# Kernel optimization log

Hardware: AMD Instinct MI355X
Metric: run time of the kernel (lower is better)

Reference implementation:

```python
import jax, jax.numpy as jnp
import numpy as np

D_MODEL = 1024
N_HEADS = 16
DK = D_MODEL // N_HEADS


def setup_inputs() -> dict:
    key = jax.random.key(0)
    k1, k2, k3, k4 = jax.random.split(key, 4)
    x = jax.random.normal(k1, (2, 2048, D_MODEL), dtype=jnp.float32)
    # torch nn.Linear stores weight as [out_features, in_features]
    W_qkv = jax.random.normal(k2, (3 * D_MODEL, D_MODEL), dtype=jnp.float32) * (1.0 / np.sqrt(D_MODEL))
    W_proj = jax.random.normal(k3, (D_MODEL, D_MODEL), dtype=jnp.float32) * (1.0 / np.sqrt(D_MODEL))
    b_proj = jax.random.normal(k4, (D_MODEL,), dtype=jnp.float32) * 0.01
    return {"x": x, "W_qkv": W_qkv, "W_proj": W_proj, "b_proj": b_proj}


def reference(x, W_qkv, W_proj, b_proj):
    B, L, D = x.shape
    qkv = x @ W_qkv.T                      # [B, L, 3D]
    q, k, v = jnp.split(qkv, 3, axis=-1)   # each [B, L, D]

    def split_heads(t):
        return t.reshape(B, L, N_HEADS, DK).transpose(0, 2, 1, 3)  # [B, H, L, dk]

    q, k, v = map(split_heads, (q, k, v))
    scale = jnp.float32(1.0 / np.sqrt(DK))
    scores = jnp.einsum('bhid,bhjd->bhij', q, k) * scale  # [B, H, L, L]
    attn = jax.nn.softmax(scores, axis=-1)
    out = jnp.einsum('bhij,bhjd->bhid', attn, v)           # [B, H, L, dk]
    out = out.transpose(0, 2, 1, 3).reshape(B, L, D)
    return out @ W_proj.T + b_proj
```

## Files before the change

### kernel.cpp

```cpp
#include <hip/hip_runtime.h>
#include <stdint.h>

typedef unsigned short ushort_t;
typedef __bf16 bf16x4 __attribute__((ext_vector_type(4)));
typedef __bf16 bf16x8 __attribute__((ext_vector_type(8)));
typedef float f32x4 __attribute__((ext_vector_type(4)));
typedef float f32x16 __attribute__((ext_vector_type(16)));
typedef unsigned short us8 __attribute__((ext_vector_type(8)));
typedef unsigned short us4v __attribute__((ext_vector_type(4)));

__device__ __forceinline__ float bf2f(ushort_t u) {
  union { uint32_t u; float f; } v; v.u = ((uint32_t)u) << 16; return v.f;
}
__device__ __forceinline__ ushort_t f2bf(float f) {
  union { float f; uint32_t u; } v; v.f = f;
  uint32_t u = v.u;
  uint32_t r = (u + 0x7FFFu + ((u >> 16) & 1u)) >> 16;
  return (ushort_t)r;
}
__device__ __forceinline__ uint32_t pkbf(float a, float b) {
  __bf16 x = (__bf16)a, y = (__bf16)b;
  uint32_t ux = __builtin_bit_cast(unsigned short, x);
  uint32_t uy = __builtin_bit_cast(unsigned short, y);
  return ux | (uy << 16);
}
__device__ __forceinline__ void gload_lds16(const void* g, void* l) {
  __builtin_amdgcn_global_load_lds(
      (const __attribute__((address_space(1))) void*)g,
      (__attribute__((address_space(3))) void*)l, 16, 0, 0);
}
__device__ __forceinline__ void tr2(const ushort_t* p, bf16x4& lo, bf16x4& hi) {
  asm volatile("ds_read_b64_tr_b16 %0, %2\n\t"
               "ds_read_b64_tr_b16 %1, %2 offset:128"
               : "=&v"(lo), "=&v"(hi)
               : "v"((const __attribute__((address_space(3))) ushort_t*)p));
}

template <typename T> __device__ __forceinline__ T to_out(float f);
template <> __device__ __forceinline__ ushort_t to_out<ushort_t>(float f) { return f2bf(f); }
template <> __device__ __forceinline__ float to_out<float>(float f) { return f; }

__global__ void f2b3_kernel(const float* __restrict__ a, ushort_t* __restrict__ ao, int na,
                            const float* __restrict__ b, ushort_t* __restrict__ bo, int nb,
                            const float* __restrict__ c, ushort_t* __restrict__ co, int nc) {
  int i = blockIdx.x * blockDim.x + threadIdx.x;
  int total = na + nb + nc;
  int stride = gridDim.x * blockDim.x;
  for (; i < total; i += stride) {
    const float* src; ushort_t* dst; int j = i;
    if (j < na) { src = a; dst = ao; }
    else if ((j -= na) < nb) { src = b; dst = bo; }
    else { j -= nb; src = c; dst = co; }
    float4 v = ((const float4*)src)[j];
    us4v o;
    o[0] = f2bf(v.x); o[1] = f2bf(v.y); o[2] = f2bf(v.z); o[3] = f2bf(v.w);
    ((us4v*)dst)[j] = o;
  }
}

template<bool BIAS, typename OT>
__global__ __launch_bounds__(256, 2) void gemm_bt(
    const ushort_t* __restrict__ A, const ushort_t* __restrict__ W,
    const float* __restrict__ bias, OT* __restrict__ C,
    int M, int N, int K)
{
  __shared__ ushort_t As[128 * 64];
  __shared__ ushort_t Bs[128 * 64];
  const int t = threadIdx.x;
  const int w = t >> 6, lane = t & 63;
  const int lg = lane >> 4, lc = lane & 15;
  const int rowbase = blockIdx.y * 128;
  const int colbase = blockIdx.x * 128;
  const int wr = (w >> 1) * 64, wc = (w & 1) * 64;

  f32x4 acc[4][4] = {};
  const int nkt = K >> 6;

  for (int kt = 0; kt < nkt; ++kt) {
#pragma unroll
    for (int i = 0; i < 4; ++i) {
      int off = (i * 256 + t) * 16;
      int row = off >> 7;
      int cb  = off & 127;
      int ec  = cb ^ ((row & 7) << 4);
      gload_lds16(A + (size_t)(rowbase + row) * K + kt * 64 + (ec >> 1),
                  (char*)As + off);
      gload_lds16(W + (size_t)(colbase + row) * K + kt * 64 + (ec >> 1),
                  (char*)Bs + off);
    }
    __syncthreads();
#pragma unroll
    for (int kk = 0; kk < 2; ++kk) {
      bf16x8 af[4], bf[4];
#pragma unroll
      for (int m = 0; m < 4; ++m) {
        int row = wr + m * 16 + lc;
        int kb  = (lg * 16 + kk * 64) ^ ((row & 7) << 4);
        af[m] = *(const bf16x8*)((const char*)As + row * 128 + kb);
        int col = wc + m * 16 + lc;
        int kb2 = (lg * 16 + kk * 64) ^ ((col & 7) << 4);
        bf[m] = *(const bf16x8*)((const char*)Bs + col * 128 + kb2);
      }
#pragma unroll
      for (int m = 0; m < 4; ++m)
#pragma unroll
        for (int n = 0; n < 4; ++n)
          acc[m][n] = __builtin_amdgcn_mfma_f32_16x16x32_bf16(af[m], bf[n],
                                                              acc[m][n], 0, 0, 0);
    }
    __syncthreads();
  }

#pragma unroll
  for (int m = 0; m < 4; ++m) {
    int r0 = rowbase + wr + m * 16 + lg * 4;
#pragma unroll
    for (int n = 0; n < 4; ++n) {
      int c0 = colbase + wc + n * 16 + lc;
      float bv = 0.f;
      if (BIAS) bv = bias[c0];
#pragma unroll
      for (int j = 0; j < 4; ++j)
        C[(size_t)(r0 + j) * N + c0] = to_out<OT>(acc[m][n][j] + bv);
    }
  }
}

__global__ __launch_bounds__(256, 2) void attn_fwd(
    const ushort_t* __restrict__ qkv, ushort_t* __restrict__ o1,
    ushort_t* __restrict__ o2, float2* __restrict__ ml)
{
  __shared__ ushort_t Ks[2][64 * 64];
  __shared__ ushort_t Vs[2][64 * 64];

  const int t = threadIdx.x, w = t >> 6, lane = t & 63;
  const int l31 = lane & 31, hi = lane >> 5;
  const int lc = lane & 15;

  const int d = blockIdx.x;
  const int qt = (d >> 3) & 15;
  const int split = (d >> 7) & 1;
  const int bh = (d & 7) * 4 + ((d >> 8) & 3);
  const int b = bh >> 4, h = bh & 15;

  const ushort_t* Qg = qkv + (size_t)(b * 2048) * 3072 + h * 64;
  const ushort_t* Kg = Qg + 1024 + (size_t)split * 1024 * 3072;
  const ushort_t* Vg = Qg + 2048 + (size_t)split * 1024 * 3072;

  auto stage_k = [&](ushort_t* Kd, int kt) {
#pragma unroll
    for (int i = 0; i < 2; ++i) {
      int off = (i * 256 + t) * 16;
      int row = off >> 7;
      int cb  = off & 127;
      int ec  = cb ^ ((row & 7) << 4);
      gload_lds16(Kg + (size_t)(kt * 64 + row) * 3072 + (ec >> 1),
                  (char*)Kd + off);
    }
  };
  int vr[2], vc0[2], vdst[2];
#pragma unroll
  for (int i = 0; i < 2; ++i) {
    int u = i * 256 + t;
    vr[i]  = u >> 3;
    vc0[i] = (u & 7) * 8;
    vdst[i] = (vc0[i] >> 4) * 2048 + (vr[i] >> 2) * 128 + (vr[i] & 3) * 32 +
              (vc0[i] & 8) * 2;
  }

  const ushort_t* qrow_p = Qg + (size_t)(qt * 128 + w * 32 + l31) * 3072;
  bf16x8 qf[4];
#pragma unroll
  for (int kk = 0; kk < 4; ++kk)
    qf[kk] = *(const bf16x8*)(qrow_p + kk * 16 + hi * 8);

  stage_k(Ks[0], 0);
#pragma unroll
  for (int i = 0; i < 2; ++i) {
    us8 v = *(const us8*)(Vg + (size_t)vr[i] * 3072 + vc0[i]);
    *(us8*)((char*)Vs[0] + vdst[i]) = v;
  }
  __syncthreads();

  f32x16 oacc0 = {}, oacc1 = {};
  float m = -1e30f, l = 0.f;
  const float SC = 0.125f * 1.44269504088896f;
  const int m16 = (lane >> 4) & 1;

  int cur = 0;
  for (int kt = 0; kt < 16; ++kt) {
    us8 vnext[2];
    if (kt < 15) {
      stage_k(Ks[cur ^ 1], kt + 1);
#pragma unroll
      for (int i = 0; i < 2; ++i)
        vnext[i] = *(const us8*)(Vg + (size_t)((kt + 1) * 64 + vr[i]) * 3072 + vc0[i]);
    }

    const ushort_t* Kc = Ks[cur];
    f32x16 s0 = {}, s1 = {};
    __builtin_amdgcn_s_setprio(1);
#pragma unroll
    for (int kk = 0; kk < 4; ++kk) {
      int cbyte = (kk * 32 + hi * 16);
      int r0 = l31, r1 = 32 + l31;
      bf16x8 kf0 = *(const bf16x8*)((const char*)Kc + r0 * 128 +
                                    (cbyte ^ ((r0 & 7) << 4)));
      bf16x8 kf1 = *(const bf16x8*)((const char*)Kc + r1 * 128 +
                                    (cbyte ^ ((r1 & 7) << 4)));
      s0 = __builtin_amdgcn_mfma_f32_32x32x16_bf16(kf0, qf[kk], s0, 0, 0, 0);
      s1 = __builtin_amdgcn_mfma_f32_32x32x16_bf16(kf1, qf[kk], s1, 0, 0, 0);
    }
    __builtin_amdgcn_s_setprio(0);

    float tm = fmaxf(s0[0], s1[0]);
#pragma unroll
    for (int i = 1; i < 16; ++i) tm = fmaxf(tm, fmaxf(s0[i], s1[i]));
    tm = fmaxf(tm, __shfl_xor(tm, 32));
    float tms = tm * SC;
    if (__any(tms > m + 8.f)) {
      float nm = fmaxf(m, tms);
      float so = __builtin_amdgcn_exp2f(m - nm);
      m = nm; l *= so;
#pragma unroll
      for (int r = 0; r < 16; ++r) {
        float sor = __shfl(so, (r & 3) + 8 * (r >> 2) + 4 * hi);
        oacc0[r] *= sor; oacc1[r] *= sor;
      }
    }
#pragma unroll
    for (int i = 0; i < 16; ++i) {
      s0[i] = __builtin_amdgcn_exp2f(__builtin_fmaf(s0[i], SC, -m));
      s1[i] = __builtin_amdgcn_exp2f(__builtin_fmaf(s1[i], SC, -m));
    }
    float rs = 0.f;
#pragma unroll
    for (int i = 0; i < 16; ++i) rs += s0[i] + s1[i];
    rs += __shfl_xor(rs, 32);
    l += rs;

    uint32_t pk0[8], pk1[8];
#pragma unroll
    for (int j = 0; j < 8; ++j) {
      pk0[j] = pkbf(s0[2 * j], s0[2 * j + 1]);
      pk1[j] = pkbf(s1[2 * j], s1[2 * j + 1]);
    }

    if (kt < 15) {
#pragma unroll
      for (int i = 0; i < 2; ++i)
        *(us8*)((char*)Vs[cur ^ 1] + vdst[i]) = vnext[i];
    }

    const ushort_t* Vc = Vs[cur];
    bf16x8 pa[4], vf[4][2];
#pragma unroll
    for (int ks = 0; ks < 4; ++ks) {
      int j0 = 4 * (ks & 1);
      uint32_t x0 = (ks < 2) ? pk0[j0]     : pk1[j0];
      uint32_t x1 = (ks < 2) ? pk0[j0 + 1] : pk1[j0 + 1];
      uint32_t y0 = (ks < 2) ? pk0[j0 + 2] : pk1[j0 + 2];
      uint32_t y1 = (ks < 2) ? pk0[j0 + 3] : pk1[j0 + 3];
      asm volatile("v_permlane32_swap_b32 %0, %1" : "+v"(x0), "+v"(y0));
      asm volatile("v_permlane32_swap_b32 %0, %1" : "+v"(x1), "+v"(y1));
      union { uint32_t du[4]; bf16x8 v; } U;
      U.du[0] = x0; U.du[1] = x1; U.du[2] = y0; U.du[3] = y1;
      pa[ks] = U.v;
#pragma unroll
      for (int nd = 0; nd < 2; ++nd) {
        bf16x4 lo, hh;
        tr2(Vc + (nd * 2 + m16) * 1024 + (4 * ks + 2 * hi) * 64 + lc * 4, lo, hh);
        vf[ks][nd] = __builtin_shufflevector(lo, hh, 0, 1, 2, 3, 4, 5, 6, 7);
      }
    }
    asm volatile("s_waitcnt lgkmcnt(0)" ::: "memory");
    __builtin_amdgcn_sched_barrier(0);
    __builtin_amdgcn_s_setprio(1);
#pragma unroll
    for (int ks = 0; ks < 4; ++ks) {
      oacc0 = __builtin_amdgcn_mfma_f32_32x32x16_bf16(pa[ks], vf[ks][0], oacc0, 0, 0, 0);
      oacc1 = __builtin_amdgcn_mfma_f32_32x32x16_bf16(pa[ks], vf[ks][1], oacc1, 0, 0, 0);
    }
    __builtin_amdgcn_s_setprio(0);

    __syncthreads();
    cur ^= 1;
  }

  ushort_t* op = split ? o2 : o1;
#pragma unroll
  for (int r = 0; r < 16; ++r) {
    int crow = (r & 3) + 8 * (r >> 2) + 4 * hi;
    int qrow = qt * 128 + w * 32 + crow;
    size_t base = ((size_t)(b * 2048 + qrow)) * 1024 + h * 64 + l31;
    op[base]      = f2bf(oacc0[r]);
    op[base + 32] = f2bf(oacc1[r]);
  }
  if (hi == 0) {
    int qrow = qt * 128 + w * 32 + l31;
    float2 v; v.x = m; v.y = l;
    ml[(size_t)split * 65536 + (size_t)(b * 2048 + qrow) * 16 + h] = v;
  }
}

__global__ void merge_kernel(ushort_t* __restrict__ o1,
                             const ushort_t* __restrict__ o2,
                             const float2* __restrict__ ml) {
  int i = blockIdx.x * blockDim.x + threadIdx.x;
  int row = i >> 7;
  int col = (i & 127) * 8;
  int h = col >> 6;
  float2 a = ml[(size_t)row * 16 + h];
  float2 c = ml[65536 + (size_t)row * 16 + h];
  float M = fmaxf(a.x, c.x);
  float w1 = __builtin_amdgcn_exp2f(a.x - M);
  float w2 = __builtin_amdgcn_exp2f(c.x - M);
  float inv = 1.f / (w1 * a.y + w2 * c.y);
  float s1 = w1 * inv, s2 = w2 * inv;
  us8 v1 = ((const us8*)o1)[i];
  us8 v2 = ((const us8*)o2)[i];
  us8 o;
#pragma unroll
  for (int j = 0; j < 8; ++j)
    o[j] = f2bf(bf2f(v1[j]) * s1 + bf2f(v2[j]) * s2);
  ((us8*)o1)[i] = o;
}

extern "C" void kernel_launch(void* const* d_in, const int* in_sizes, int n_in,
                              void* d_out, int out_size, void* d_ws, size_t ws_size,
                              hipStream_t stream) {
  const float* x     = (const float*)d_in[0];
  const float* Wqkv  = (const float*)d_in[1];
  const float* Wproj = (const float*)d_in[2];
  const float* bproj = (const float*)d_in[3];
  float* out = (float*)d_out;

  ushort_t* qkv   = (ushort_t*)d_ws;
  ushort_t* aout  = qkv   + (size_t)4096 * 3072;
  ushort_t* xb    = aout  + (size_t)4096 * 1024;
  ushort_t* wqb   = xb    + (size_t)4096 * 1024;
  ushort_t* wpb   = wqb   + (size_t)3072 * 1024;
  float2*   mlbuf = (float2*)(wpb + (size_t)1024 * 1024);

  dim3 blk(256);
  f2b3_kernel<<<2048, blk, 0, stream>>>(x, xb, 4096 * 1024 / 4,
                                        Wqkv, wqb, 3072 * 1024 / 4,
                                        Wproj, wpb, 1024 * 1024 / 4);

  gemm_bt<false, ushort_t><<<dim3(24, 32), blk, 0, stream>>>(
      xb, wqb, nullptr, qkv, 4096, 3072, 1024);
  attn_fwd<<<dim3(1024), blk, 0, stream>>>(qkv, aout, xb, mlbuf);
  merge_kernel<<<2048, blk, 0, stream>>>(aout, xb, mlbuf);
  gemm_bt<true, float><<<dim3(8, 32), blk, 0, stream>>>(
      aout, wpb, bproj, out, 4096, 1024, 1024);
}
```

Before: 127.0 us.

## Enlarge attention blocks to 512 threads with 256-query tiles sharing K/V

The attention kernel now runs 8 waves per block over 256 query rows instead of 4 waves over 128, so each staged K/V tile in LDS serves twice as many queries. The grid halves to 512 blocks and the block-index mapping to (batch·head, split, query tile) is rewritten to match. Each thread now issues one K and one V load per tile instead of two, which halves the global-to-LDS traffic per query. The cost is fewer, larger blocks, a 4-per-CU launch bound that caps register use, and a heavier barrier across 8 waves.

New measurement: 121.6 us. -4.2%, faster.

```diff
diff --git a/kernel.cpp b/kernel.cpp
--- a/kernel.cpp
+++ b/kernel.cpp
@@ -126,7 +126,7 @@
   }
 }
 
-__global__ __launch_bounds__(256, 2) void attn_fwd(
+__global__ __launch_bounds__(512, 4) void attn_fwd(
     const ushort_t* __restrict__ qkv, ushort_t* __restrict__ o1,
     ushort_t* __restrict__ o2, float2* __restrict__ ml)
 {
@@ -138,9 +138,9 @@
   const int lc = lane & 15;
 
   const int d = blockIdx.x;
-  const int qt = (d >> 3) & 15;
-  const int split = (d >> 7) & 1;
-  const int bh = (d & 7) * 4 + ((d >> 8) & 3);
+  const int qt = (d >> 3) & 7;
+  const int bhs = (d & 7) * 8 + (d >> 6);
+  const int bh = bhs >> 1, split = bhs & 1;
   const int b = bh >> 4, h = bh & 15;
 
   const ushort_t* Qg = qkv + (size_t)(b * 2048) * 3072 + h * 64;
@@ -148,37 +148,28 @@
   const ushort_t* Vg = Qg + 2048 + (size_t)split * 1024 * 3072;
 
   auto stage_k = [&](ushort_t* Kd, int kt) {
-#pragma unroll
-    for (int i = 0; i < 2; ++i) {
-      int off = (i * 256 + t) * 16;
-      int row = off >> 7;
-      int cb  = off & 127;
-      int ec  = cb ^ ((row & 7) << 4);
-      gload_lds16(Kg + (size_t)(kt * 64 + row) * 3072 + (ec >> 1),
-                  (char*)Kd + off);
-    }
+    int off = t * 16;
+    int row = off >> 7;
+    int cb  = off & 127;
+    int ec  = cb ^ ((row & 7) << 4);
+    gload_lds16(Kg + (size_t)(kt * 64 + row) * 3072 + (ec >> 1),
+                (char*)Kd + off);
   };
-  int vr[2], vc0[2], vdst[2];
-#pragma unroll
-  for (int i = 0; i < 2; ++i) {
-    int u = i * 256 + t;
-    vr[i]  = u >> 3;
-    vc0[i] = (u & 7) * 8;
-    vdst[i] = (vc0[i] >> 4) * 2048 + (vr[i] >> 2) * 128 + (vr[i] & 3) * 32 +
-              (vc0[i] & 8) * 2;
-  }
-
-  const ushort_t* qrow_p = Qg + (size_t)(qt * 128 + w * 32 + l31) * 3072;
+  const int vr  = t >> 3;
+  const int vc0 = (t & 7) * 8;
+  const int vdst = (vc0 >> 4) * 2048 + (vr >> 2) * 128 + (vr & 3) * 32 +
+                   (vc0 & 8) * 2;
+
+  const ushort_t* qrow_p = Qg + (size_t)(qt * 256 + w * 32 + l31) * 3072;
   bf16x8 qf[4];
 #pragma unroll
   for (int kk = 0; kk < 4; ++kk)
     qf[kk] = *(const bf16x8*)(qrow_p + kk * 16 + hi * 8);
 
   stage_k(Ks[0], 0);
-#pragma unroll
-  for (int i = 0; i < 2; ++i) {
-    us8 v = *(const us8*)(Vg + (size_t)vr[i] * 3072 + vc0[i]);
-    *(us8*)((char*)Vs[0] + vdst[i]) = v;
+  {
+    us8 v = *(const us8*)(Vg + (size_t)vr * 3072 + vc0);
+    *(us8*)((char*)Vs[0] + vdst) = v;
   }
   __syncthreads();
 
@@ -189,12 +180,10 @@
 
   int cur = 0;
   for (int kt = 0; kt < 16; ++kt) {
-    us8 vnext[2];
+    us8 vnext;
     if (kt < 15) {
       stage_k(Ks[cur ^ 1], kt + 1);
-#pragma unroll
-      for (int i = 0; i < 2; ++i)
-        vnext[i] = *(const us8*)(Vg + (size_t)((kt + 1) * 64 + vr[i]) * 3072 + vc0[i]);
+      vnext = *(const us8*)(Vg + (size_t)((kt + 1) * 64 + vr) * 3072 + vc0);
     }
 
     const ushort_t* Kc = Ks[cur];
@@ -246,11 +235,8 @@
       pk1[j] = pkbf(s1[2 * j], s1[2 * j + 1]);
     }
 
-    if (kt < 15) {
-#pragma unroll
-      for (int i = 0; i < 2; ++i)
-        *(us8*)((char*)Vs[cur ^ 1] + vdst[i]) = vnext[i];
-    }
+    if (kt < 15)
+      *(us8*)((char*)Vs[cur ^ 1] + vdst) = vnext;
 
     const ushort_t* Vc = Vs[cur];
     bf16x8 pa[4], vf[4][2];
@@ -291,13 +277,13 @@
 #pragma unroll
   for (int r = 0; r < 16; ++r) {
     int crow = (r & 3) + 8 * (r >> 2) + 4 * hi;
-    int qrow = qt * 128 + w * 32 + crow;
+    int qrow = qt * 256 + w * 32 + crow;
     size_t base = ((size_t)(b * 2048 + qrow)) * 1024 + h * 64 + l31;
     op[base]      = f2bf(oacc0[r]);
     op[base + 32] = f2bf(oacc1[r]);
   }
   if (hi == 0) {
-    int qrow = qt * 128 + w * 32 + l31;
+    int qrow = qt * 256 + w * 32 + l31;
     float2 v; v.x = m; v.y = l;
     ml[(size_t)split * 65536 + (size_t)(b * 2048 + qrow) * 16 + h] = v;
   }
@@ -349,7 +335,7 @@
 
   gemm_bt<false, ushort_t><<<dim3(24, 32), blk, 0, stream>>>(
       xb, wqb, nullptr, qkv, 4096, 3072, 1024);
-  attn_fwd<<<dim3(1024), blk, 0, stream>>>(qkv, aout, xb, mlbuf);
+  attn_fwd<<<dim3(512), dim3(512), 0, stream>>>(qkv, aout, xb, mlbuf);
   merge_kernel<<<2048, blk, 0, stream>>>(aout, xb, mlbuf);
   gemm_bt<true, float><<<dim3(8, 32), blk, 0, stream>>>(
       aout, wpb, bproj, out, 4096, 1024, 1024);
```
